# Optimization experiments

Hardware: AMD Instinct MI355X
Metric: run time of the kernel (lower is better)

The kernel has to match this reference:

```python
import jax, jax.numpy as jnp
import numpy as np

PATCH = 14  # dinov2 patch size
LN_EPS = 1e-5


def setup_inputs() -> dict:
    key = jax.random.key(0)
    ks = jax.random.split(key, 6)
    Nb, P, E, Hd = 4096, 5476, 1024, 128  # boxes, patches (74*74), embed_dim, hidden_dim
    return {
        "patch_tokens": jax.random.normal(ks[0], (1, P, E), dtype=jnp.float32),
        "bboxes": jax.random.randint(ks[1], (Nb, 4), 0, 1036, dtype=jnp.int32),
        "H": 1036,
        "W": 1036,
        "W1": jax.random.normal(ks[2], (E, Hd), dtype=jnp.float32) * 0.02,
        "b1": jnp.zeros((Hd,), dtype=jnp.float32),
        "gamma": jnp.ones((Hd,), dtype=jnp.float32),
        "beta": jnp.zeros((Hd,), dtype=jnp.float32),
        "W2": jax.random.normal(ks[3], (Hd, Hd), dtype=jnp.float32) * 0.02,
        "b2": jnp.zeros((Hd,), dtype=jnp.float32),
    }


def _roi_pool(patch_tokens, bboxes, H, W):
    """Vectorized equivalent of VisionEncoder.roi_pool_patches.

    patch_tokens: (1, nph*npw, E); bboxes: (Nb, 4) int pixel coords.
    Returns (Nb, E) mean of patch tokens inside each box.
    """
    nph, npw = H // PATCH, W // PATCH
    Nb = bboxes.shape[0]
    x1, y1, x2, y2 = (bboxes[:, 0], bboxes[:, 1], bboxes[:, 2], bboxes[:, 3])
    f32 = jnp.float32
    # int() truncation in torch == astype(int32) for non-negative values
    px1 = (x1.astype(f32) / W * npw).astype(jnp.int32)
    px2 = (x2.astype(f32) / W * npw).astype(jnp.int32)
    py1 = (y1.astype(f32) / H * nph).astype(jnp.int32)
    py2 = (y2.astype(f32) / H * nph).astype(jnp.int32)
    px1 = jnp.clip(px1, 0, npw - 1)
    px2 = jnp.maximum(px1 + 1, jnp.minimum(px2, npw))
    py1 = jnp.clip(py1, 0, nph - 1)
    py2 = jnp.maximum(py1 + 1, jnp.minimum(py2, nph))
    # Box membership masks over the patch grid (ragged gather expressed densely)
    ay = jnp.arange(nph, dtype=jnp.int32)
    ax = jnp.arange(npw, dtype=jnp.int32)
    my = (ay[None, :] >= py1[:, None]) & (ay[None, :] < py2[:, None])  # (Nb, nph)
    mx = (ax[None, :] >= px1[:, None]) & (ax[None, :] < px2[:, None])  # (Nb, npw)
    mask = (my[:, :, None] & mx[:, None, :]).reshape(Nb, nph * npw)
    mask = mask.astype(patch_tokens.dtype)
    counts = mask.sum(axis=-1, keepdims=True)  # always >= 1 by construction
    pooled = (mask @ patch_tokens[0]) / counts  # (Nb, E)
    return pooled


def _projection(x, W1, b1, gamma, beta, W2, b2):
    h = x @ W1 + b1
    mu = h.mean(axis=-1, keepdims=True)
    var = ((h - mu) ** 2).mean(axis=-1, keepdims=True)
    h = (h - mu) * jax.lax.rsqrt(var + LN_EPS) * gamma + beta
    h = jax.nn.relu(h)
    return h @ W2 + b2


def reference(patch_tokens, bboxes, H, W, W1, b1, gamma, beta, W2, b2):
    pooled = _roi_pool(patch_tokens, bboxes, H, W)
    return _projection(pooled, W1, b1, gamma, beta, W2, b2)
```

## Files before the change

### kernel.cpp

```cpp
#include <hip/hip_runtime.h>


#define HD 128

__device__ __forceinline__ int decode_dim(const int* p, int fallback) {
    if (p == nullptr) return fallback;
    int vi = *p;
    if (vi >= 1 && vi <= 1000000) return vi;
    float vf = __int_as_float(vi);
    if (vf >= 1.0f && vf <= 1000000.0f) return (int)vf;
    return fallback;
}

__attribute__((noinline, optnone))
__device__ int coord_map(int x, int W, int n) {
    double rd = 1.0 / (double)W;
    float r = (float)rd;
    double qd = (double)x * (double)r;
    float q = (float)qd;
    double pd = (double)q * (double)n;
    float p = (float)pd;
    return (int)p;
}

__global__ __launch_bounds__(256) void gemm_u_kernel(
    const float* __restrict__ T, const float* __restrict__ W1,
    float* __restrict__ U, int P, int E)
{
    __shared__ float As[32][64];
    __shared__ float Bs[32][HD];

    int t  = threadIdx.x;
    int tc = t & 31;
    int tr = t >> 5;
    int row0 = blockIdx.x * 64;
    int ks   = blockIdx.y;
    int kchunk = E >> 2;
    int kbase  = ks * kchunk;
    float* Uo = U + (size_t)ks * (size_t)P * HD;

    float acc[8][4];
#pragma unroll
    for (int r = 0; r < 8; ++r)
#pragma unroll
        for (int j = 0; j < 4; ++j) acc[r][j] = 0.f;

    int arow = t >> 2;
    int akq  = (t & 3) * 8;
    int brow = t >> 5;
    int bc   = (t & 31) * 4;

    for (int kt = 0; kt < kchunk; kt += 32) {
        int k0 = kbase + kt;
        {
            int rg = row0 + arow; if (rg >= P) rg = P - 1;
            const float* tp = T + (size_t)rg * E + k0 + akq;
            float4 v0 = *(const float4*)tp;
            float4 v1 = *(const float4*)(tp + 4);
            As[akq + 0][arow] = v0.x; As[akq + 1][arow] = v0.y;
            As[akq + 2][arow] = v0.z; As[akq + 3][arow] = v0.w;
            As[akq + 4][arow] = v1.x; As[akq + 5][arow] = v1.y;
            As[akq + 6][arow] = v1.z; As[akq + 7][arow] = v1.w;
        }
#pragma unroll
        for (int i = 0; i < 4; ++i) {
            int kk = brow + i * 8;
            *(float4*)&Bs[kk][bc] =
                *(const float4*)&W1[(size_t)(k0 + kk) * HD + bc];
        }
        __syncthreads();

#pragma unroll
        for (int kk = 0; kk < 32; ++kk) {
            float4 a0 = *(const float4*)&As[kk][tr * 8];
            float4 a1 = *(const float4*)&As[kk][tr * 8 + 4];
            float4 b  = *(const float4*)&Bs[kk][tc * 4];
            float av[8] = {a0.x, a0.y, a0.z, a0.w, a1.x, a1.y, a1.z, a1.w};
            float bv[4] = {b.x, b.y, b.z, b.w};
#pragma unroll
            for (int r = 0; r < 8; ++r)
#pragma unroll
                for (int j = 0; j < 4; ++j)
                    acc[r][j] += av[r] * bv[j];
        }
        __syncthreads();
    }

#pragma unroll
    for (int r = 0; r < 8; ++r) {
        int p = row0 + tr * 8 + r;
        if (p < P) {
            float4 v = make_float4(acc[r][0], acc[r][1], acc[r][2], acc[r][3]);
            *(float4*)&Uo[(size_t)p * HD + tc * 4] = v;
        }
    }
}

__global__ __launch_bounds__(256) void prefix_x_kernel(
    const float* __restrict__ U, float* __restrict__ S,
    int P, int npw, int nph)
{
    extern __shared__ float tile[];
    int t = threadIdx.x;
    int y = blockIdx.x;
    int rowlen = npw * HD;
    size_t ubase = (size_t)y * rowlen;
    size_t ustride = (size_t)P * HD;

    for (int j = t; j < rowlen / 4; j += 256) {
        const float4* p0 = (const float4*)(U + ubase) + j;
        const float4* p1 = (const float4*)(U + ustride + ubase) + j;
        const float4* p2 = (const float4*)(U + 2 * ustride + ubase) + j;
        const float4* p3 = (const float4*)(U + 3 * ustride + ubase) + j;
        float4 a = *p0, b = *p1, c = *p2, d = *p3;
        float4 s = make_float4(a.x + b.x + c.x + d.x, a.y + b.y + c.y + d.y,
                               a.z + b.z + c.z + d.z, a.w + b.w + c.w + d.w);
        ((float4*)tile)[j] = s;
    }
    __syncthreads();

    if (t < HD) {
        int c = t;
        size_t srow = (size_t)(y + 1) * (npw + 1) * HD;
        S[srow + c] = 0.f;
        float acc = 0.f;
        for (int x = 0; x < npw; ++x) {
            acc += tile[x * HD + c];
            S[srow + (size_t)(x + 1) * HD + c] = acc;
        }
    }
}

__global__ __launch_bounds__(256) void prefix_y_kernel(
    float* __restrict__ S, int npw, int nph)
{
    extern __shared__ float tile[];
    int t = threadIdx.x;
    int x = blockIdx.x;
    size_t stride = (size_t)(npw + 1) * HD;
    size_t base = (size_t)x * HD;

    for (int j = t; j < nph * HD; j += 256) {
        int y = j >> 7, c = j & 127;
        tile[j] = S[base + (size_t)(y + 1) * stride + c];
    }
    __syncthreads();

    if (t < HD) {
        int c = t;
        S[base + c] = 0.f;
        float acc = 0.f;
        for (int y = 0; y < nph; ++y) {
            acc += tile[y * HD + c];
            S[base + (size_t)(y + 1) * stride + c] = acc;
        }
    }
}

__global__ __launch_bounds__(256) void pool_proj_kernel(
    const float* __restrict__ S, const int* __restrict__ bboxes,
    const int* __restrict__ pH, const int* __restrict__ pW,
    const float* __restrict__ b1, const float* __restrict__ gamma,
    const float* __restrict__ beta, const float* __restrict__ W2,
    const float* __restrict__ b2, float* __restrict__ out,
    int Nb, int npw, int nph, int fbW, int fbH)
{
    __shared__ float hs[16][HD + 1];
    __shared__ float Bs[32][HD];
    __shared__ int   cI11[16], cI12[16], cI21[16], cI22[16];
    __shared__ float cCnt[16];
    __shared__ float mu_s[16], rs_s[16];

    int t = threadIdx.x;
    int c = t & 127;
    int rh = t >> 7;
    int row0 = blockIdx.x * 16;

    if (t < 16) {
        int b = row0 + t; if (b >= Nb) b = Nb - 1;
        int x1 = bboxes[b * 4 + 0];
        int y1 = bboxes[b * 4 + 1];
        int x2 = bboxes[b * 4 + 2];
        int y2 = bboxes[b * 4 + 3];
        int Wi = decode_dim(pW, fbW);
        int Hi = decode_dim(pH, fbH);
        int px1 = coord_map(x1, Wi, npw);
        int px2 = coord_map(x2, Wi, npw);
        int py1 = coord_map(y1, Hi, nph);
        int py2 = coord_map(y2, Hi, nph);
        px1 = min(max(px1, 0), npw - 1);
        px2 = max(px1 + 1, min(px2, npw));
        py1 = min(max(py1, 0), nph - 1);
        py2 = max(py1 + 1, min(py2, nph));
        int st = npw + 1;
        cI11[t] = (py1 * st + px1) * HD;
        cI12[t] = (py1 * st + px2) * HD;
        cI21[t] = (py2 * st + px1) * HD;
        cI22[t] = (py2 * st + px2) * HD;
        cCnt[t] = (float)((py2 - py1) * (px2 - px1));
    }
    __syncthreads();

    float bias1 = b1[c];
    float hv[8];
#pragma unroll
    for (int r = 0; r < 8; ++r) {
        int row = rh * 8 + r;
        float s = S[cI22[row] + c] - S[cI12[row] + c]
                - S[cI21[row] + c] + S[cI11[row] + c];
        hv[r] = s / cCnt[row] + bias1;
        hs[row][c] = hv[r];
    }
    __syncthreads();

    if (t < 16) {
        float m = 0.f;
#pragma unroll 8
        for (int i = 0; i < HD; ++i) m += hs[t][i];
        m *= (1.0f / HD);
        float v = 0.f;
#pragma unroll 8
        for (int i = 0; i < HD; ++i) { float d = hs[t][i] - m; v += d * d; }
        v *= (1.0f / HD);
        mu_s[t] = m;
        rs_s[t] = rsqrtf(v + 1e-5f);
    }
    __syncthreads();

    float g = gamma[c], be = beta[c];
#pragma unroll
    for (int r = 0; r < 8; ++r) {
        int row = rh * 8 + r;
        float x = (hv[r] - mu_s[row]) * rs_s[row] * g + be;
        hs[row][c] = fmaxf(x, 0.f);
    }
    __syncthreads();

    float bias2 = b2[c];
    float acc2[8];
#pragma unroll
    for (int r = 0; r < 8; ++r) acc2[r] = bias2;
    for (int k0 = 0; k0 < HD; k0 += 32) {
#pragma unroll
        for (int i = 0; i < 16; ++i) {
            int idx = t + i * 256;
            int kk = idx >> 7, cc = idx & 127;
            Bs[kk][cc] = W2[(size_t)(k0 + kk) * HD + cc];
        }
        __syncthreads();
#pragma unroll
        for (int kk = 0; kk < 32; ++kk) {
            float bv = Bs[kk][c];
#pragma unroll
            for (int r = 0; r < 8; ++r)
                acc2[r] += hs[rh * 8 + r][k0 + kk] * bv;
        }
        __syncthreads();
    }

#pragma unroll
    for (int r = 0; r < 8; ++r) {
        int rg = row0 + rh * 8 + r;
        if (rg < Nb) out[(size_t)rg * HD + c] = acc2[r];
    }
}

extern "C" void kernel_launch(void* const* d_in, const int* in_sizes, int n_in,
                              void* d_out, int out_size, void* d_ws, size_t ws_size,
                              hipStream_t stream) {
    int iT = 0, iB = 1, iH = 2, iW = 3, iW1 = 4, ib1 = 5, ig = 6, ibe = 7,
        iW2 = 8, ib2 = 9;
    bool has_scalars = (n_in >= 10 && in_sizes[2] == 1 && in_sizes[3] == 1);
    if (!has_scalars) { iW1 = 2; ib1 = 3; ig = 4; ibe = 5; iW2 = 6; ib2 = 7; }

    const float* tokens = (const float*)d_in[iT];
    const int*   bboxes = (const int*)d_in[iB];
    const int*   pH     = has_scalars ? (const int*)d_in[iH] : nullptr;
    const int*   pW     = has_scalars ? (const int*)d_in[iW] : nullptr;
    const float* W1     = (const float*)d_in[iW1];
    const float* b1     = (const float*)d_in[ib1];
    const float* gamma  = (const float*)d_in[ig];
    const float* beta   = (const float*)d_in[ibe];
    const float* W2     = (const float*)d_in[iW2];
    const float* b2     = (const float*)d_in[ib2];
    float* out = (float*)d_out;

    int Hd = in_sizes[ib1];
    int E  = in_sizes[iW1] / Hd;
    int Nb = in_sizes[iB] / 4;
    int P  = in_sizes[iT] / E;
    int npw = 1;
    while ((npw + 1) * (npw + 1) <= P) ++npw;
    int nph = P / npw;
    (void)out_size; (void)ws_size;

    float* S = (float*)d_ws;
    size_t s_elems = ((size_t)(nph + 1) * (npw + 1) * HD + 255) & ~(size_t)255;
    float* U = S + s_elems;

    int mtiles = (P + 63) / 64;
    gemm_u_kernel<<<dim3(mtiles, 4), dim3(256), 0, stream>>>(
        tokens, W1, U, P, E);
    prefix_x_kernel<<<dim3(nph), dim3(256), (size_t)npw * HD * 4, stream>>>(
        U, S, P, npw, nph);
    prefix_y_kernel<<<dim3(npw + 1), dim3(256), (size_t)nph * HD * 4, stream>>>(
        S, npw, nph);
    pool_proj_kernel<<<dim3((Nb + 15) / 16), dim3(256), 0, stream>>>(
        S, bboxes, pH, pW, b1, gamma, beta, W2, b2, out, Nb, npw, nph,
        14 * npw, 14 * nph);
}
```

Before: 143.0 us.

## Raise split-K to 8, split prefix scans by channel halves, parallelize LayerNorm stats

```diff
diff --git a/kernel.cpp b/kernel.cpp
--- a/kernel.cpp
+++ b/kernel.cpp
@@ -2,6 +2,7 @@
 
 
 #define HD 128
+#define SPLITK 8
 
 __device__ __forceinline__ int decode_dim(const int* p, int fallback) {
     if (p == nullptr) return fallback;
@@ -27,7 +28,7 @@
     const float* __restrict__ T, const float* __restrict__ W1,
     float* __restrict__ U, int P, int E)
 {
-    __shared__ float As[32][64];
+    __shared__ float As[32][65];
     __shared__ float Bs[32][HD];
 
     int t  = threadIdx.x;
@@ -35,7 +36,7 @@
     int tr = t >> 5;
     int row0 = blockIdx.x * 64;
     int ks   = blockIdx.y;
-    int kchunk = E >> 2;
+    int kchunk = E >> 3;
     int kbase  = ks * kchunk;
     float* Uo = U + (size_t)ks * (size_t)P * HD;
 
@@ -103,29 +104,31 @@
     extern __shared__ float tile[];
     int t = threadIdx.x;
     int y = blockIdx.x;
-    int rowlen = npw * HD;
-    size_t ubase = (size_t)y * rowlen;
+    int ch0 = blockIdx.y * 64;
     size_t ustride = (size_t)P * HD;
-
-    for (int j = t; j < rowlen / 4; j += 256) {
-        const float4* p0 = (const float4*)(U + ubase) + j;
-        const float4* p1 = (const float4*)(U + ustride + ubase) + j;
-        const float4* p2 = (const float4*)(U + 2 * ustride + ubase) + j;
-        const float4* p3 = (const float4*)(U + 3 * ustride + ubase) + j;
-        float4 a = *p0, b = *p1, c = *p2, d = *p3;
-        float4 s = make_float4(a.x + b.x + c.x + d.x, a.y + b.y + c.y + d.y,
-                               a.z + b.z + c.z + d.z, a.w + b.w + c.w + d.w);
-        ((float4*)tile)[j] = s;
-    }
-    __syncthreads();
-
-    if (t < HD) {
+    size_t ubase = (size_t)y * npw * HD + ch0;
+
+    int nj = npw * 16;
+    for (int j = t; j < nj; j += 256) {
+        int x = j >> 4, cq = (j & 15) * 4;
+        size_t off = ubase + (size_t)x * HD + cq;
+        float4 s = *(const float4*)(U + off);
+#pragma unroll
+        for (int p = 1; p < SPLITK; ++p) {
+            float4 v = *(const float4*)(U + (size_t)p * ustride + off);
+            s.x += v.x; s.y += v.y; s.z += v.z; s.w += v.w;
+        }
+        *(float4*)&tile[x * 64 + cq] = s;
+    }
+    __syncthreads();
+
+    if (t < 64) {
         int c = t;
-        size_t srow = (size_t)(y + 1) * (npw + 1) * HD;
+        size_t srow = (size_t)(y + 1) * (npw + 1) * HD + ch0;
         S[srow + c] = 0.f;
         float acc = 0.f;
         for (int x = 0; x < npw; ++x) {
-            acc += tile[x * HD + c];
+            acc += tile[x * 64 + c];
             S[srow + (size_t)(x + 1) * HD + c] = acc;
         }
     }
@@ -137,21 +140,24 @@
     extern __shared__ float tile[];
     int t = threadIdx.x;
     int x = blockIdx.x;
+    int ch0 = blockIdx.y * 64;
     size_t stride = (size_t)(npw + 1) * HD;
-    size_t base = (size_t)x * HD;
-
-    for (int j = t; j < nph * HD; j += 256) {
-        int y = j >> 7, c = j & 127;
-        tile[j] = S[base + (size_t)(y + 1) * stride + c];
-    }
-    __syncthreads();
-
-    if (t < HD) {
+    size_t base = (size_t)x * HD + ch0;
+
+    int nj = nph * 16;
+    for (int j = t; j < nj; j += 256) {
+        int y = j >> 4, cq = (j & 15) * 4;
+        *(float4*)&tile[y * 64 + cq] =
+            *(const float4*)(S + base + (size_t)(y + 1) * stride + cq);
+    }
+    __syncthreads();
+
+    if (t < 64) {
         int c = t;
         S[base + c] = 0.f;
         float acc = 0.f;
         for (int y = 0; y < nph; ++y) {
-            acc += tile[y * HD + c];
+            acc += tile[y * 64 + c];
             S[base + (size_t)(y + 1) * stride + c] = acc;
         }
     }
@@ -167,6 +173,7 @@
 {
     __shared__ float hs[16][HD + 1];
     __shared__ float Bs[32][HD];
+    __shared__ float red_s[16][17], red_q[16][17];
     __shared__ int   cI11[16], cI12[16], cI21[16], cI22[16];
     __shared__ float cCnt[16];
     __shared__ float mu_s[16], rs_s[16];
@@ -213,15 +220,24 @@
     }
     __syncthreads();
 
+    {
+        int sr = t & 15;
+        int sg = t >> 4;
+        float ps = 0.f, pq = 0.f;
+#pragma unroll
+        for (int i = 0; i < 8; ++i) {
+            float v = hs[sr][sg * 8 + i];
+            ps += v; pq += v * v;
+        }
+        red_s[sr][sg] = ps; red_q[sr][sg] = pq;
+    }
+    __syncthreads();
     if (t < 16) {
-        float m = 0.f;
-#pragma unroll 8
-        for (int i = 0; i < HD; ++i) m += hs[t][i];
-        m *= (1.0f / HD);
-        float v = 0.f;
-#pragma unroll 8
-        for (int i = 0; i < HD; ++i) { float d = hs[t][i] - m; v += d * d; }
-        v *= (1.0f / HD);
+        float s = 0.f, q = 0.f;
+#pragma unroll
+        for (int i = 0; i < 16; ++i) { s += red_s[t][i]; q += red_q[t][i]; }
+        float m = s * (1.0f / HD);
+        float v = q * (1.0f / HD) - m * m;
         mu_s[t] = m;
         rs_s[t] = rsqrtf(v + 1e-5f);
     }
@@ -299,11 +315,11 @@
     float* U = S + s_elems;
 
     int mtiles = (P + 63) / 64;
-    gemm_u_kernel<<<dim3(mtiles, 4), dim3(256), 0, stream>>>(
+    gemm_u_kernel<<<dim3(mtiles, SPLITK), dim3(256), 0, stream>>>(
         tokens, W1, U, P, E);
-    prefix_x_kernel<<<dim3(nph), dim3(256), (size_t)npw * HD * 4, stream>>>(
+    prefix_x_kernel<<<dim3(nph, 2), dim3(256), (size_t)npw * 64 * 4, stream>>>(
         U, S, P, npw, nph);
-    prefix_y_kernel<<<dim3(npw + 1), dim3(256), (size_t)nph * HD * 4, stream>>>(
+    prefix_y_kernel<<<dim3(npw + 1, 2), dim3(256), (size_t)nph * 64 * 4, stream>>>(
         S, npw, nph);
     pool_proj_kernel<<<dim3((Nb + 15) / 16), dim3(256), 0, stream>>>(
         S, bboxes, pH, pW, b1, gamma, beta, W2, b2, out, Nb, npw, nph,
```

New measurement: 137.8 us. -3.6%, faster.
